# Performance work log

Hardware: AMD Instinct MI355X
Metric: run time of the kernel (lower is better)

## Reference

```python
import jax, jax.numpy as jnp
import numpy as np
from jax import lax

BETA = 1e-07
LAMBDA_TV = 1e-08


def _resize_bilinear_ac(x, out_h, out_w):
    """Bilinear resize with align_corners=True, NCHW layout (matches F.interpolate)."""
    B, C, H, W = x.shape
    ys = jnp.arange(out_h, dtype=jnp.float32) * ((H - 1) / max(out_h - 1, 1))
    xs = jnp.arange(out_w, dtype=jnp.float32) * ((W - 1) / max(out_w - 1, 1))
    y0 = jnp.floor(ys).astype(jnp.int32); y1 = jnp.minimum(y0 + 1, H - 1)
    x0 = jnp.floor(xs).astype(jnp.int32); x1 = jnp.minimum(x0 + 1, W - 1)
    wy = (ys - y0.astype(jnp.float32))[:, None]   # [out_h,1]
    wx = (xs - x0.astype(jnp.float32))[None, :]   # [1,out_w]
    r0 = x[:, :, y0, :]; r1 = x[:, :, y1, :]      # [B,C,out_h,W]
    top = r0[:, :, :, x0] * (1.0 - wx) + r0[:, :, :, x1] * wx
    bot = r1[:, :, :, x0] * (1.0 - wx) + r1[:, :, :, x1] * wx
    return top * (1.0 - wy) + bot * wy


def _levelset_loss(output, target):
    B = output.shape[0]
    # pcentroid computed under no_grad in torch -> stop_gradient here
    num = jnp.einsum('bthw,bchw->btc', target, output)
    den = jnp.sum(output, axis=(2, 3))                       # [B,C]
    pcent = lax.stop_gradient(num / den[:, None, :])          # [B,T,C]
    plevel = target[:, :, None, :, :] - pcent[:, :, :, None, None]  # [B,T,C,H,W]
    return jnp.sum(plevel * plevel * output[:, None]) / B


def _gradient_loss2d(output):
    B = output.shape[0]
    dH = jnp.abs(output[:, :, 1:, :] - output[:, :, :-1, :])
    dW = jnp.abs(output[:, :, :, 1:] - output[:, :, :, :-1])
    return (jnp.sum(dH) + jnp.sum(dW)) / B


def _nonlocal_tv_loss(f_output, f_sem):
    B, Cs, H, W = f_sem.shape
    N = H * W
    fo = _resize_bilinear_ac(f_output, H, W)                  # [B,C,H,W]
    C = fo.shape[1]
    # F.normalize(f_sem, dim=1) (eps=1e-12)
    norm = jnp.sqrt(jnp.sum(f_sem * f_sem, axis=1, keepdims=True))
    sem = f_sem / jnp.maximum(norm, 1e-12)
    sem_f = sem.reshape(B, Cs, N)
    # tau[b,r,p] = relu(<sem_r, sem_p>); normalized by global spatial max per (b,r)
    tau = jax.nn.relu(jnp.einsum('bcr,bcp->brp', sem_f, sem_f))  # [B,N,N]
    tau_max = jnp.max(tau, axis=2, keepdims=True)
    tau_n = tau / (tau_max + 1e-05)
    # torch.matmul(dL[B,C,H,W], tau[B,1,H,W]) summed over everything reduces to
    # sum_{i,k,j} dL[b,c,i,k] * tau[b,k,j] = sum_k (sum_i dL[b,c,i,k]) * (sum_j tau[b,k,j])
    t = tau_n.reshape(B, N, H, W).sum(axis=3)                 # [B,N,H] row-sums of tau
    of = fo.reshape(B, C, N)
    # dL[b,c,r,h,w] = |out_r - out_{(h,w)}| (penalty='l1')
    dL = jnp.abs(of[:, :, :, None, None] - fo[:, :, None, :, :])  # [B,C,N,H,W]
    A = dL.sum(axis=3)                                         # [B,C,N,W] sum over rows i
    return jnp.einsum('bcrk,brk->', A, t) / B


def setup_inputs() -> dict:
    key = jax.random.key(0)
    k1, k2, k3, k4 = jax.random.split(key, 4)
    return {
        'output': jax.random.uniform(k1, (4, 21, 512, 512), dtype=jnp.float32),
        'target': jax.random.uniform(k2, (4, 3, 512, 512), dtype=jnp.float32),
        'f_sem': jax.random.normal(k3, (4, 256, 32, 32), dtype=jnp.float32),
        'f_output': jax.random.uniform(k4, (4, 21, 64, 64), dtype=jnp.float32),
        'use_NonLocal_TV': 1,
    }


def reference(output, target, f_sem, f_output, use_NonLocal_TV):
    loss_LS = _levelset_loss(output, target)
    if use_NonLocal_TV:
        loss_TV = _nonlocal_tv_loss(f_output, f_sem) * LAMBDA_TV
    else:
        loss_TV = _gradient_loss2d(output) * LAMBDA_TV
    loss_MS = (loss_LS + loss_TV) * BETA
    return (loss_LS * BETA, loss_TV * BETA, loss_MS)
```

## Files before the change

kernel.cpp:

```cpp
#include <hip/hip_runtime.h>

#define BETA_F   1e-7f
#define LAMBDA_F 1e-8f

#define NB   4
#define CO   21
#define HWSZ 262144
#define NBC  84
#define NPIX 1024

#define OFF_FO    0
#define OFF_GSUM  86016
#define OFF_INVN  (86016 + 131072)
#define OFF_RMAX  (217088 + 4096)
#define OFF_LS    (221184 + 4096)
#define OFF_ACC   (225280 + 588)
#define ZERO_START OFF_RMAX
#define ZERO_COUNT (4096 + 588 + 4)

__global__ void k_zero(float* __restrict__ ws) {
    int i = blockIdx.x * 256 + threadIdx.x;
    if (i < ZERO_COUNT) ws[ZERO_START + i] = 0.f;
}

__global__ __launch_bounds__(256) void k_ls(const float* __restrict__ outp,
                                            const float* __restrict__ tgt,
                                            float* __restrict__ ws) {
    const int slice = blockIdx.x, bc = blockIdx.y;
    const int b = bc / 21;
    const int tid = threadIdx.x;
    const float4* o4 = (const float4*)(outp + (size_t)bc * HWSZ + slice * 8192);
    const float4* t4 = (const float4*)(tgt + (size_t)b * (3 * HWSZ) + slice * 8192);
    float n0 = 0, n1 = 0, n2 = 0, q0 = 0, q1 = 0, q2 = 0, dn = 0;
    for (int i = tid; i < 2048; i += 256) {
        float4 o  = o4[i];
        float4 ta = t4[i];
        float4 tb = t4[i + 65536];
        float4 tc = t4[i + 131072];
        dn += o.x + o.y + o.z + o.w;
        n0 += ta.x*o.x + ta.y*o.y + ta.z*o.z + ta.w*o.w;
        q0 += ta.x*ta.x*o.x + ta.y*ta.y*o.y + ta.z*ta.z*o.z + ta.w*ta.w*o.w;
        n1 += tb.x*o.x + tb.y*o.y + tb.z*o.z + tb.w*o.w;
        q1 += tb.x*tb.x*o.x + tb.y*tb.y*o.y + tb.z*tb.z*o.z + tb.w*tb.w*o.w;
        n2 += tc.x*o.x + tc.y*o.y + tc.z*o.z + tc.w*o.w;
        q2 += tc.x*tc.x*o.x + tc.y*tc.y*o.y + tc.z*tc.z*o.z + tc.w*tc.w*o.w;
    }
    float vals[7] = {n0, n1, n2, q0, q1, q2, dn};
    __shared__ float red[4][7];
    #pragma unroll
    for (int j = 0; j < 7; ++j) {
        float v = vals[j];
        #pragma unroll
        for (int off = 32; off; off >>= 1) v += __shfl_xor(v, off);
        if ((tid & 63) == 0) red[tid >> 6][j] = v;
    }
    __syncthreads();
    if (tid < 7) {
        float s = red[0][tid] + red[1][tid] + red[2][tid] + red[3][tid];
        atomicAdd(&ws[OFF_LS + bc * 7 + tid], s);
    }
}

__global__ void k_resize(const float* __restrict__ fo_in, float* __restrict__ ws) {
    const int bc = blockIdx.x;
    const int tid = threadIdx.x;
    const int oy = tid >> 5, ox = tid & 31;
    const float R = 63.0f / 31.0f;
    float sy = oy * R, sx = ox * R;
    int y0 = (int)sy, x0 = (int)sx;
    int y1 = min(y0 + 1, 63), x1 = min(x0 + 1, 63);
    float wy = sy - (float)y0, wx = sx - (float)x0;
    const float* im = fo_in + bc * 4096;
    float v00 = im[y0 * 64 + x0], v01 = im[y0 * 64 + x1];
    float v10 = im[y1 * 64 + x0], v11 = im[y1 * 64 + x1];
    float top = v00 * (1.f - wx) + v01 * wx;
    float bot = v10 * (1.f - wx) + v11 * wx;
    ws[OFF_FO + bc * NPIX + tid] = top * (1.f - wy) + bot * wy;
}

__global__ void k_norm(const float* __restrict__ fsem, float* __restrict__ ws) {
    const int b = blockIdx.x >> 4, pg = blockIdx.x & 15;
    const int p0 = pg * 64;
    const int pi = threadIdx.x & 63, cg = threadIdx.x >> 6;
    float s = 0.f;
    for (int c = cg; c < 256; c += 4) {
        float v = fsem[(b * 256 + c) * 1024 + p0 + pi];
        s += v * v;
    }
    __shared__ float red[4][64];
    red[cg][pi] = s;
    __syncthreads();
    if (threadIdx.x < 64) {
        float t = red[0][threadIdx.x] + red[1][threadIdx.x] +
                  red[2][threadIdx.x] + red[3][threadIdx.x];
        ws[OFF_INVN + b * 1024 + p0 + threadIdx.x] = 1.f / fmaxf(sqrtf(t), 1e-12f);
    }
}

__device__ __forceinline__ int swz(int p4, int k) {
    int s = (p4 >> 1) | ((p4 & 1) << 4);
    return s ^ (k & 7);
}

__global__ __launch_bounds__(256) void k_gram(const float* __restrict__ fsem,
                                              float* __restrict__ ws) {
    const int ct = blockIdx.x, rt = blockIdx.y, b = blockIdx.z;
    const int r0 = rt * 128, c0 = ct * 128;
    const int tid = threadIdx.x;
    __shared__ float4 As4[64 * 32];
    __shared__ float4 Bs4[64 * 32];
    __shared__ float  gsum_s[512];
    __shared__ int    rmax_s[128];
    for (int i = tid; i < 512; i += 256) gsum_s[i] = 0.f;
    if (tid < 128) rmax_s[tid] = 0;

    const int tr = tid >> 4, tc = tid & 15;
    float acc[8][8];
    #pragma unroll
    for (int i = 0; i < 8; ++i)
        #pragma unroll
        for (int j = 0; j < 8; ++j) acc[i][j] = 0.f;

    const int kl = tid >> 5, p4s = tid & 31;
    for (int kk = 0; kk < 4; ++kk) {
        __syncthreads();
        #pragma unroll
        for (int q = 0; q < 8; ++q) {
            int k = kl + q * 8;
            const float* srcA = &fsem[(b * 256 + kk * 64 + k) * 1024 + r0 + p4s * 4];
            const float* srcB = &fsem[(b * 256 + kk * 64 + k) * 1024 + c0 + p4s * 4];
            float4 va = *(const float4*)srcA;
            float4 vb = *(const float4*)srcB;
            int sl = swz(p4s, k);
            As4[k * 32 + sl] = va;
            Bs4[k * 32 + sl] = vb;
        }
        __syncthreads();
        #pragma unroll 4
        for (int k = 0; k < 64; ++k) {
            int k7 = k & 7;
            float4 a0 = As4[k * 32 + (tr ^ k7)];
            float4 a1 = As4[k * 32 + ((tr ^ k7) | 16)];
            float4 b0 = Bs4[k * 32 + (tc ^ k7)];
            float4 b1 = Bs4[k * 32 + ((tc ^ k7) | 16)];
            float a[8]  = {a0.x, a0.y, a0.z, a0.w, a1.x, a1.y, a1.z, a1.w};
            float bb[8] = {b0.x, b0.y, b0.z, b0.w, b1.x, b1.y, b1.z, b1.w};
            #pragma unroll
            for (int i = 0; i < 8; ++i)
                #pragma unroll
                for (int j = 0; j < 8; ++j)
                    acc[i][j] += a[i] * bb[j];
        }
    }

    float ir[8], ic[8];
    #pragma unroll
    for (int i = 0; i < 8; ++i) {
        ir[i] = ws[OFF_INVN + b * 1024 + r0 + tr * 8 + i];
        ic[i] = ws[OFF_INVN + b * 1024 + c0 + tc * 8 + i];
    }
    const int g = tc >> 2;
    #pragma unroll
    for (int i = 0; i < 8; ++i) {
        float s = 0.f, m = 0.f;
        #pragma unroll
        for (int j = 0; j < 8; ++j) {
            float v = fmaxf(acc[i][j], 0.f) * ir[i] * ic[j];
            s += v;
            m = fmaxf(m, v);
        }
        int row = tr * 8 + i;
        atomicAdd(&gsum_s[row * 4 + g], s);
        atomicMax(&rmax_s[row], __float_as_int(m));
    }
    __syncthreads();
    for (int i = tid; i < 512; i += 256) {
        int row = i >> 2, gg = i & 3;
        ws[OFF_GSUM + (b * 1024 + r0 + row) * 32 + ct * 4 + gg] = gsum_s[i];
    }
    if (tid < 128)
        atomicMax((int*)&ws[OFF_RMAX + b * 1024 + r0 + tid], rmax_s[tid]);
}

__global__ __launch_bounds__(256) void k_tv(const float* __restrict__ ws,
                                            float* __restrict__ acc_out) {
    const int bc = blockIdx.y;
    const int b = bc / 21;
    const int tid = threadIdx.x;
    __shared__ float4 fo4[256];
    const float4* src = (const float4*)(ws + OFF_FO + bc * NPIX);
    fo4[tid] = src[tid];
    __syncthreads();
    const int r = blockIdx.x * 256 + tid;
    const float v = ((const float*)fo4)[r];
    float ak[32];
    #pragma unroll
    for (int k = 0; k < 32; ++k) ak[k] = 0.f;
    #pragma unroll 4
    for (int h = 0; h < 32; ++h) {
        #pragma unroll
        for (int k4 = 0; k4 < 8; ++k4) {
            float4 f = fo4[h * 8 + k4];
            ak[k4 * 4 + 0] += fabsf(v - f.x);
            ak[k4 * 4 + 1] += fabsf(v - f.y);
            ak[k4 * 4 + 2] += fabsf(v - f.z);
            ak[k4 * 4 + 3] += fabsf(v - f.w);
        }
    }
    const float rm = ws[OFF_RMAX + b * 1024 + r];
    const float inv = 1.f / (rm + 1e-5f);
    const float* t = ws + OFF_GSUM + (b * 1024 + r) * 32;
    float dot = 0.f;
    #pragma unroll
    for (int k = 0; k < 32; ++k) dot += ak[k] * t[k];
    float part = dot * inv;
    #pragma unroll
    for (int off = 32; off; off >>= 1) part += __shfl_xor(part, off);
    __shared__ float red[4];
    if ((tid & 63) == 0) red[tid >> 6] = part;
    __syncthreads();
    if (tid == 0) atomicAdd(acc_out, red[0] + red[1] + red[2] + red[3]);
}

__global__ void k_combine(const float* __restrict__ ws, float* __restrict__ out) {
    const int tid = threadIdx.x;
    float v = 0.f;
    if (tid < NBC) {
        const float* p = ws + OFF_LS + tid * 7;
        float den = p[6];
        v = (p[3] + p[4] + p[5]) - (p[0]*p[0] + p[1]*p[1] + p[2]*p[2]) / den;
    }
    #pragma unroll
    for (int off = 32; off; off >>= 1) v += __shfl_xor(v, off);
    __shared__ float red[2];
    if ((tid & 63) == 0) red[tid >> 6] = v;
    __syncthreads();
    if (tid == 0) {
        float lsv = (red[0] + red[1]) * 0.25f;
        float tvv = ws[OFF_ACC] * 0.25f;
        out[0] = lsv * BETA_F;
        out[1] = tvv * LAMBDA_F * BETA_F;
        out[2] = (lsv + tvv * LAMBDA_F) * BETA_F;
    }
}

extern "C" void kernel_launch(void* const* d_in, const int* in_sizes, int n_in,
                              void* d_out, int out_size, void* d_ws, size_t ws_size,
                              hipStream_t stream) {
    const float* output   = (const float*)d_in[0];
    const float* target   = (const float*)d_in[1];
    const float* f_sem    = (const float*)d_in[2];
    const float* f_output = (const float*)d_in[3];
    float* ws  = (float*)d_ws;
    float* out = (float*)d_out;

    hipLaunchKernelGGL(k_zero,    dim3((ZERO_COUNT + 255) / 256), dim3(256), 0, stream, ws);
    hipLaunchKernelGGL(k_ls,      dim3(32, 84), dim3(256),  0, stream, output, target, ws);
    hipLaunchKernelGGL(k_resize,  dim3(84),     dim3(1024), 0, stream, f_output, ws);
    hipLaunchKernelGGL(k_norm,    dim3(64),     dim3(256),  0, stream, f_sem, ws);
    hipLaunchKernelGGL(k_gram,    dim3(8, 8, 4), dim3(256), 0, stream, f_sem, ws);
    hipLaunchKernelGGL(k_tv,      dim3(4, 84),  dim3(256),  0, stream, ws, ws + OFF_ACC);
    hipLaunchKernelGGL(k_combine, dim3(1),      dim3(128),  0, stream, ws, out);
}
```

Before: 242.0 us.

## Merge prep kernels and co-schedule gram with levelset reduction in one launch

Folds the zeroing, bilinear resize and norm kernels into a single block-dispatched prep kernel. It also merges the gram-matrix GEMM and the memory-bound levelset reduction into one kernel, with the gram blocks first and the reduction blocks after, so the compute-bound and bandwidth-bound work can overlap on the GPU. Together this cuts seven launches to four. The cost is that every block of the merged kernel reserves the full 68KB of shared memory, which may lower occupancy for the reduction blocks, and the levelset loop gains an unroll-by-2 hint.

```diff
diff --git a/kernel.cpp b/kernel.cpp
--- a/kernel.cpp
+++ b/kernel.cpp
@@ -3,8 +3,6 @@
 #define BETA_F   1e-7f
 #define LAMBDA_F 1e-8f
 
-#define NB   4
-#define CO   21
 #define HWSZ 262144
 #define NBC  84
 #define NPIX 1024
@@ -18,82 +16,46 @@
 #define ZERO_START OFF_RMAX
 #define ZERO_COUNT (4096 + 588 + 4)
 
-__global__ void k_zero(float* __restrict__ ws) {
-    int i = blockIdx.x * 256 + threadIdx.x;
-    if (i < ZERO_COUNT) ws[ZERO_START + i] = 0.f;
-}
-
-__global__ __launch_bounds__(256) void k_ls(const float* __restrict__ outp,
-                                            const float* __restrict__ tgt,
-                                            float* __restrict__ ws) {
-    const int slice = blockIdx.x, bc = blockIdx.y;
-    const int b = bc / 21;
-    const int tid = threadIdx.x;
-    const float4* o4 = (const float4*)(outp + (size_t)bc * HWSZ + slice * 8192);
-    const float4* t4 = (const float4*)(tgt + (size_t)b * (3 * HWSZ) + slice * 8192);
-    float n0 = 0, n1 = 0, n2 = 0, q0 = 0, q1 = 0, q2 = 0, dn = 0;
-    for (int i = tid; i < 2048; i += 256) {
-        float4 o  = o4[i];
-        float4 ta = t4[i];
-        float4 tb = t4[i + 65536];
-        float4 tc = t4[i + 131072];
-        dn += o.x + o.y + o.z + o.w;
-        n0 += ta.x*o.x + ta.y*o.y + ta.z*o.z + ta.w*o.w;
-        q0 += ta.x*ta.x*o.x + ta.y*ta.y*o.y + ta.z*ta.z*o.z + ta.w*ta.w*o.w;
-        n1 += tb.x*o.x + tb.y*o.y + tb.z*o.z + tb.w*o.w;
-        q1 += tb.x*tb.x*o.x + tb.y*tb.y*o.y + tb.z*tb.z*o.z + tb.w*tb.w*o.w;
-        n2 += tc.x*o.x + tc.y*o.y + tc.z*o.z + tc.w*o.w;
-        q2 += tc.x*tc.x*o.x + tc.y*tc.y*o.y + tc.z*tc.z*o.z + tc.w*tc.w*o.w;
-    }
-    float vals[7] = {n0, n1, n2, q0, q1, q2, dn};
-    __shared__ float red[4][7];
-    #pragma unroll
-    for (int j = 0; j < 7; ++j) {
-        float v = vals[j];
-        #pragma unroll
-        for (int off = 32; off; off >>= 1) v += __shfl_xor(v, off);
-        if ((tid & 63) == 0) red[tid >> 6][j] = v;
-    }
-    __syncthreads();
-    if (tid < 7) {
-        float s = red[0][tid] + red[1][tid] + red[2][tid] + red[3][tid];
-        atomicAdd(&ws[OFF_LS + bc * 7 + tid], s);
-    }
-}
-
-__global__ void k_resize(const float* __restrict__ fo_in, float* __restrict__ ws) {
-    const int bc = blockIdx.x;
-    const int tid = threadIdx.x;
-    const int oy = tid >> 5, ox = tid & 31;
-    const float R = 63.0f / 31.0f;
-    float sy = oy * R, sx = ox * R;
-    int y0 = (int)sy, x0 = (int)sx;
-    int y1 = min(y0 + 1, 63), x1 = min(x0 + 1, 63);
-    float wy = sy - (float)y0, wx = sx - (float)x0;
-    const float* im = fo_in + bc * 4096;
-    float v00 = im[y0 * 64 + x0], v01 = im[y0 * 64 + x1];
-    float v10 = im[y1 * 64 + x0], v11 = im[y1 * 64 + x1];
-    float top = v00 * (1.f - wx) + v01 * wx;
-    float bot = v10 * (1.f - wx) + v11 * wx;
-    ws[OFF_FO + bc * NPIX + tid] = top * (1.f - wy) + bot * wy;
-}
-
-__global__ void k_norm(const float* __restrict__ fsem, float* __restrict__ ws) {
-    const int b = blockIdx.x >> 4, pg = blockIdx.x & 15;
-    const int p0 = pg * 64;
-    const int pi = threadIdx.x & 63, cg = threadIdx.x >> 6;
-    float s = 0.f;
-    for (int c = cg; c < 256; c += 4) {
-        float v = fsem[(b * 256 + c) * 1024 + p0 + pi];
-        s += v * v;
-    }
-    __shared__ float red[4][64];
-    red[cg][pi] = s;
-    __syncthreads();
-    if (threadIdx.x < 64) {
-        float t = red[0][threadIdx.x] + red[1][threadIdx.x] +
-                  red[2][threadIdx.x] + red[3][threadIdx.x];
-        ws[OFF_INVN + b * 1024 + p0 + threadIdx.x] = 1.f / fmaxf(sqrtf(t), 1e-12f);
+__global__ __launch_bounds__(256) void k_prep(const float* __restrict__ fo_in,
+                                              const float* __restrict__ fsem,
+                                              float* __restrict__ ws) {
+    const int bid = blockIdx.x, tid = threadIdx.x;
+    if (bid < 19) {
+        int i = bid * 256 + tid;
+        if (i < ZERO_COUNT) ws[ZERO_START + i] = 0.f;
+    } else if (bid < 103) {
+        const int bc = bid - 19;
+        const float* im = fo_in + bc * 4096;
+        for (int p = tid; p < 1024; p += 256) {
+            const int oy = p >> 5, ox = p & 31;
+            const float R = 63.0f / 31.0f;
+            float sy = oy * R, sx = ox * R;
+            int y0 = (int)sy, x0 = (int)sx;
+            int y1 = min(y0 + 1, 63), x1 = min(x0 + 1, 63);
+            float wy = sy - (float)y0, wx = sx - (float)x0;
+            float v00 = im[y0 * 64 + x0], v01 = im[y0 * 64 + x1];
+            float v10 = im[y1 * 64 + x0], v11 = im[y1 * 64 + x1];
+            float top = v00 * (1.f - wx) + v01 * wx;
+            float bot = v10 * (1.f - wx) + v11 * wx;
+            ws[OFF_FO + bc * NPIX + p] = top * (1.f - wy) + bot * wy;
+        }
+    } else {
+        const int blk = bid - 103;
+        const int b = blk >> 4, pg = blk & 15;
+        const int p0 = pg * 64;
+        const int pi = tid & 63, cg = tid >> 6;
+        float s = 0.f;
+        for (int c = cg; c < 256; c += 4) {
+            float v = fsem[(b * 256 + c) * 1024 + p0 + pi];
+            s += v * v;
+        }
+        __shared__ float red[4][64];
+        red[cg][pi] = s;
+        __syncthreads();
+        if (tid < 64) {
+            float t = red[0][tid] + red[1][tid] + red[2][tid] + red[3][tid];
+            ws[OFF_INVN + b * 1024 + p0 + tid] = 1.f / fmaxf(sqrtf(t), 1e-12f);
+        }
     }
 }
 
@@ -102,84 +64,126 @@
     return s ^ (k & 7);
 }
 
-__global__ __launch_bounds__(256) void k_gram(const float* __restrict__ fsem,
+__global__ __launch_bounds__(256) void k_main(const float* __restrict__ outp,
+                                              const float* __restrict__ tgt,
+                                              const float* __restrict__ fsem,
                                               float* __restrict__ ws) {
-    const int ct = blockIdx.x, rt = blockIdx.y, b = blockIdx.z;
-    const int r0 = rt * 128, c0 = ct * 128;
+    __shared__ __align__(16) char smem[68096];
     const int tid = threadIdx.x;
-    __shared__ float4 As4[64 * 32];
-    __shared__ float4 Bs4[64 * 32];
-    __shared__ float  gsum_s[512];
-    __shared__ int    rmax_s[128];
-    for (int i = tid; i < 512; i += 256) gsum_s[i] = 0.f;
-    if (tid < 128) rmax_s[tid] = 0;
-
-    const int tr = tid >> 4, tc = tid & 15;
-    float acc[8][8];
-    #pragma unroll
-    for (int i = 0; i < 8; ++i)
-        #pragma unroll
-        for (int j = 0; j < 8; ++j) acc[i][j] = 0.f;
-
-    const int kl = tid >> 5, p4s = tid & 31;
-    for (int kk = 0; kk < 4; ++kk) {
+
+    if (blockIdx.x < 256) {
+        float4* As4    = (float4*)smem;
+        float4* Bs4    = (float4*)(smem + 32768);
+        float*  gsum_s = (float*)(smem + 65536);
+        int*    rmax_s = (int*)(smem + 67584);
+        const int bid = blockIdx.x;
+        const int ct = bid & 7, rt = (bid >> 3) & 7, b = bid >> 6;
+        const int r0 = rt * 128, c0 = ct * 128;
+        for (int i = tid; i < 512; i += 256) gsum_s[i] = 0.f;
+        if (tid < 128) rmax_s[tid] = 0;
+
+        const int tr = tid >> 4, tc = tid & 15;
+        float acc[8][8];
+        #pragma unroll
+        for (int i = 0; i < 8; ++i)
+            #pragma unroll
+            for (int j = 0; j < 8; ++j) acc[i][j] = 0.f;
+
+        const int kl = tid >> 5, p4s = tid & 31;
+        for (int kk = 0; kk < 4; ++kk) {
+            __syncthreads();
+            #pragma unroll
+            for (int q = 0; q < 8; ++q) {
+                int k = kl + q * 8;
+                const float* srcA = &fsem[(b * 256 + kk * 64 + k) * 1024 + r0 + p4s * 4];
+                const float* srcB = &fsem[(b * 256 + kk * 64 + k) * 1024 + c0 + p4s * 4];
+                float4 va = *(const float4*)srcA;
+                float4 vb = *(const float4*)srcB;
+                int sl = swz(p4s, k);
+                As4[k * 32 + sl] = va;
+                Bs4[k * 32 + sl] = vb;
+            }
+            __syncthreads();
+            #pragma unroll 4
+            for (int k = 0; k < 64; ++k) {
+                int k7 = k & 7;
+                float4 a0 = As4[k * 32 + (tr ^ k7)];
+                float4 a1 = As4[k * 32 + ((tr ^ k7) | 16)];
+                float4 b0 = Bs4[k * 32 + (tc ^ k7)];
+                float4 b1 = Bs4[k * 32 + ((tc ^ k7) | 16)];
+                float a[8]  = {a0.x, a0.y, a0.z, a0.w, a1.x, a1.y, a1.z, a1.w};
+                float bb[8] = {b0.x, b0.y, b0.z, b0.w, b1.x, b1.y, b1.z, b1.w};
+                #pragma unroll
+                for (int i = 0; i < 8; ++i)
+                    #pragma unroll
+                    for (int j = 0; j < 8; ++j)
+                        acc[i][j] += a[i] * bb[j];
+            }
+        }
+
+        float ir[8], ic[8];
+        #pragma unroll
+        for (int i = 0; i < 8; ++i) {
+            ir[i] = ws[OFF_INVN + b * 1024 + r0 + tr * 8 + i];
+            ic[i] = ws[OFF_INVN + b * 1024 + c0 + tc * 8 + i];
+        }
+        const int g = tc >> 2;
+        #pragma unroll
+        for (int i = 0; i < 8; ++i) {
+            float s = 0.f, m = 0.f;
+            #pragma unroll
+            for (int j = 0; j < 8; ++j) {
+                float v = fmaxf(acc[i][j], 0.f) * ir[i] * ic[j];
+                s += v;
+                m = fmaxf(m, v);
+            }
+            int row = tr * 8 + i;
+            atomicAdd(&gsum_s[row * 4 + g], s);
+            atomicMax(&rmax_s[row], __float_as_int(m));
+        }
         __syncthreads();
-        #pragma unroll
-        for (int q = 0; q < 8; ++q) {
-            int k = kl + q * 8;
-            const float* srcA = &fsem[(b * 256 + kk * 64 + k) * 1024 + r0 + p4s * 4];
-            const float* srcB = &fsem[(b * 256 + kk * 64 + k) * 1024 + c0 + p4s * 4];
-            float4 va = *(const float4*)srcA;
-            float4 vb = *(const float4*)srcB;
-            int sl = swz(p4s, k);
-            As4[k * 32 + sl] = va;
-            Bs4[k * 32 + sl] = vb;
+        for (int i = tid; i < 512; i += 256) {
+            int row = i >> 2, gg = i & 3;
+            ws[OFF_GSUM + (b * 1024 + r0 + row) * 32 + ct * 4 + gg] = gsum_s[i];
+        }
+        if (tid < 128)
+            atomicMax((int*)&ws[OFF_RMAX + b * 1024 + r0 + tid], rmax_s[tid]);
+    } else {
+        float (*red)[7] = (float (*)[7])smem;
+        const int blk = blockIdx.x - 256;
+        const int slice = blk & 31, bc = blk >> 5;
+        const int b = bc / 21;
+        const float4* o4 = (const float4*)(outp + (size_t)bc * HWSZ + slice * 8192);
+        const float4* t4 = (const float4*)(tgt + (size_t)b * (3 * HWSZ) + slice * 8192);
+        float n0 = 0, n1 = 0, n2 = 0, q0 = 0, q1 = 0, q2 = 0, dn = 0;
+        #pragma unroll 2
+        for (int i = tid; i < 2048; i += 256) {
+            float4 o  = o4[i];
+            float4 ta = t4[i];
+            float4 tb = t4[i + 65536];
+            float4 tc = t4[i + 131072];
+            dn += o.x + o.y + o.z + o.w;
+            n0 += ta.x*o.x + ta.y*o.y + ta.z*o.z + ta.w*o.w;
+            q0 += ta.x*ta.x*o.x + ta.y*ta.y*o.y + ta.z*ta.z*o.z + ta.w*ta.w*o.w;
+            n1 += tb.x*o.x + tb.y*o.y + tb.z*o.z + tb.w*o.w;
+            q1 += tb.x*tb.x*o.x + tb.y*tb.y*o.y + tb.z*tb.z*o.z + tb.w*tb.w*o.w;
+            n2 += tc.x*o.x + tc.y*o.y + tc.z*o.z + tc.w*o.w;
+            q2 += tc.x*tc.x*o.x + tc.y*tc.y*o.y + tc.z*tc.z*o.z + tc.w*tc.w*o.w;
+        }
+        float vals[7] = {n0, n1, n2, q0, q1, q2, dn};
+        #pragma unroll
+        for (int j = 0; j < 7; ++j) {
+            float v = vals[j];
+            #pragma unroll
+            for (int off = 32; off; off >>= 1) v += __shfl_xor(v, off);
+            if ((tid & 63) == 0) red[tid >> 6][j] = v;
         }
         __syncthreads();
-        #pragma unroll 4
-        for (int k = 0; k < 64; ++k) {
-            int k7 = k & 7;
-            float4 a0 = As4[k * 32 + (tr ^ k7)];
-            float4 a1 = As4[k * 32 + ((tr ^ k7) | 16)];
-            float4 b0 = Bs4[k * 32 + (tc ^ k7)];
-            float4 b1 = Bs4[k * 32 + ((tc ^ k7) | 16)];
-            float a[8]  = {a0.x, a0.y, a0.z, a0.w, a1.x, a1.y, a1.z, a1.w};
-            float bb[8] = {b0.x, b0.y, b0.z, b0.w, b1.x, b1.y, b1.z, b1.w};
-            #pragma unroll
-            for (int i = 0; i < 8; ++i)
-                #pragma unroll
-                for (int j = 0; j < 8; ++j)
-                    acc[i][j] += a[i] * bb[j];
-        }
-    }
-
-    float ir[8], ic[8];
-    #pragma unroll
-    for (int i = 0; i < 8; ++i) {
-        ir[i] = ws[OFF_INVN + b * 1024 + r0 + tr * 8 + i];
-        ic[i] = ws[OFF_INVN + b * 1024 + c0 + tc * 8 + i];
-    }
-    const int g = tc >> 2;
-    #pragma unroll
-    for (int i = 0; i < 8; ++i) {
-        float s = 0.f, m = 0.f;
-        #pragma unroll
-        for (int j = 0; j < 8; ++j) {
-            float v = fmaxf(acc[i][j], 0.f) * ir[i] * ic[j];
-            s += v;
-            m = fmaxf(m, v);
-        }
-        int row = tr * 8 + i;
-        atomicAdd(&gsum_s[row * 4 + g], s);
-        atomicMax(&rmax_s[row], __float_as_int(m));
-    }
-    __syncthreads();
-    for (int i = tid; i < 512; i += 256) {
-        int row = i >> 2, gg = i & 3;
-        ws[OFF_GSUM + (b * 1024 + r0 + row) * 32 + ct * 4 + gg] = gsum_s[i];
-    }
-    if (tid < 128)
-        atomicMax((int*)&ws[OFF_RMAX + b * 1024 + r0 + tid], rmax_s[tid]);
+        if (tid < 7) {
+            float s = red[0][tid] + red[1][tid] + red[2][tid] + red[3][tid];
+            atomicAdd(&ws[OFF_LS + bc * 7 + tid], s);
+        }
+    }
 }
 
 __global__ __launch_bounds__(256) void k_tv(const float* __restrict__ ws,
@@ -254,11 +258,8 @@
     float* ws  = (float*)d_ws;
     float* out = (float*)d_out;
 
-    hipLaunchKernelGGL(k_zero,    dim3((ZERO_COUNT + 255) / 256), dim3(256), 0, stream, ws);
-    hipLaunchKernelGGL(k_ls,      dim3(32, 84), dim3(256),  0, stream, output, target, ws);
-    hipLaunchKernelGGL(k_resize,  dim3(84),     dim3(1024), 0, stream, f_output, ws);
-    hipLaunchKernelGGL(k_norm,    dim3(64),     dim3(256),  0, stream, f_sem, ws);
-    hipLaunchKernelGGL(k_gram,    dim3(8, 8, 4), dim3(256), 0, stream, f_sem, ws);
-    hipLaunchKernelGGL(k_tv,      dim3(4, 84),  dim3(256),  0, stream, ws, ws + OFF_ACC);
-    hipLaunchKernelGGL(k_combine, dim3(1),      dim3(128),  0, stream, ws, out);
-}
+    hipLaunchKernelGGL(k_prep,    dim3(167),    dim3(256), 0, stream, f_output, f_sem, ws);
+    hipLaunchKernelGGL(k_main,    dim3(2944),   dim3(256), 0, stream, output, target, f_sem, ws);
+    hipLaunchKernelGGL(k_tv,      dim3(4, 84),  dim3(256), 0, stream, ws, ws + OFF_ACC);
+    hipLaunchKernelGGL(k_combine, dim3(1),      dim3(128), 0, stream, ws, out);
+}
```

Result: faster. 224.5 us (-7.2%).
